# Performance work log

Measured on AMD Instinct MI355X. Metric: run time of the kernel, lower is better.

## Reference

```python
import jax, jax.numpy as jnp
import numpy as np

B, F = 65536, 64
H1, H2 = 64, 64  # linear_layers = [64, 64]
NEG_SLOPE = 0.05


def leaky(x):
    return jnp.where(x >= 0, x, NEG_SLOPE * x)


def setup_inputs() -> dict:
    key = jax.random.key(0)
    ks = jax.random.split(key, 7)
    x = jax.random.normal(ks[0], (B, 1, F), dtype=jnp.float32)
    # Per-feature stacked weights (PyTorch default init scale ~ 1/sqrt(fan_in))
    W1 = jax.random.uniform(ks[1], (F, H1), jnp.float32, -1.0, 1.0)          # Linear(1, H1) weight, fan_in=1
    b1 = jax.random.uniform(ks[2], (F, H1), jnp.float32, -1.0, 1.0)
    s2 = 1.0 / np.sqrt(H1)
    W2 = jax.random.uniform(ks[3], (F, H2, H1), jnp.float32, -s2, s2)        # Linear(H1, H2)
    b2 = jax.random.uniform(ks[4], (F, H2), jnp.float32, -s2, s2)
    s3 = 1.0 / np.sqrt(H2)
    W3 = jax.random.uniform(ks[5], (F, H2), jnp.float32, -s3, s3)            # Linear(H2, 1) weight
    b3 = jax.random.uniform(ks[6], (F,), jnp.float32, -s3, s3)
    return {"x": x, "W1": W1, "b1": b1, "W2": W2, "b2": b2, "W3": W3, "b3": b3}


def reference(x, W1, b1, W2, b2, W3, b3):
    # x: [B, 1, F]; apply an independent tiny 2-layer MLP to each scalar feature.
    xs = x[:, 0, :]                                   # [B, F]
    h = leaky(xs[:, :, None] * W1[None] + b1[None])   # [B, F, H1]
    h = leaky(jnp.einsum('bfh,fgh->bfg', h, W2) + b2[None])  # [B, F, H2]
    y = jnp.einsum('bfg,fg->bf', h, W3) + b3[None]    # [B, F]
    return y[:, None, :]                              # [B, 1, F], same shape as x
```

## Files before the change

kernel.cpp:

```cpp
#include <hip/hip_runtime.h>

typedef _Float16 half8  __attribute__((ext_vector_type(8)));
typedef _Float16 half4v __attribute__((ext_vector_type(4)));
typedef float    floatx4 __attribute__((ext_vector_type(4)));

static constexpr int BR      = 256;
static constexpr int FG      = 16;
static constexpr int XP      = 17;
static constexpr int THREADS = 256;
#define NEG_SLOPE 0.05f

__global__ __launch_bounds__(256)
void w2_half_kernel(const float* __restrict__ W2, _Float16* __restrict__ W2h) {
    int i = (blockIdx.x * 256 + threadIdx.x) * 4;
    floatx4 v = *reinterpret_cast<const floatx4*>(W2 + i);
    half4v h;
    h[0] = (_Float16)v[0]; h[1] = (_Float16)v[1];
    h[2] = (_Float16)v[2]; h[3] = (_Float16)v[3];
    *reinterpret_cast<half4v*>(W2h + i) = h;
}

__global__ __launch_bounds__(THREADS, 3)
void mft_kernel(const float* __restrict__ x,
                const float* __restrict__ W1,
                const float* __restrict__ b1,
                const _Float16* __restrict__ W2h,
                const float* __restrict__ b2,
                const float* __restrict__ W3,
                const float* __restrict__ b3,
                float* __restrict__ y) {
    __shared__ float xl[BR * XP];
    __shared__ float yl[BR * XP];

    const int tid   = threadIdx.x;
    const int fg    = blockIdx.x & 3;
    const int chunk = blockIdx.x >> 2;
    const int gbase = chunk * (BR * 64) + fg * FG;

    #pragma unroll
    for (int k = 0; k < (BR * FG) / (THREADS * 4); ++k) {
        int i  = (k * THREADS + tid) * 4;
        int r  = i >> 4;
        int fi = i & 15;
        floatx4 v = *reinterpret_cast<const floatx4*>(x + gbase + r * 64 + fi);
        xl[r * XP + fi + 0] = v[0];
        xl[r * XP + fi + 1] = v[1];
        xl[r * XP + fi + 2] = v[2];
        xl[r * XP + fi + 3] = v[3];
    }
    __syncthreads();

    const int lane = tid & 63;
    const int wave = tid >> 6;
    const int l15  = lane & 15;
    const int lg   = lane >> 4;

    for (int fi = 0; fi < FG; ++fi) {
        const int f = fg * FG + fi;
        const _Float16* w2f = W2h + f * 4096;

        half8 afrag[4][2];
        #pragma unroll
        for (int m = 0; m < 4; ++m)
            #pragma unroll
            for (int s = 0; s < 2; ++s)
                afrag[m][s] = *reinterpret_cast<const half8*>(
                    w2f + (m * 16 + l15) * 64 + s * 32 + lg * 8);

        floatx4 w1a[2][2], b1a[2][2];
        #pragma unroll
        for (int s = 0; s < 2; ++s) {
            const int ko = s * 32 + lg * 8;
            w1a[s][0] = *reinterpret_cast<const floatx4*>(W1 + f * 64 + ko);
            w1a[s][1] = *reinterpret_cast<const floatx4*>(W1 + f * 64 + ko + 4);
            b1a[s][0] = *reinterpret_cast<const floatx4*>(b1 + f * 64 + ko);
            b1a[s][1] = *reinterpret_cast<const floatx4*>(b1 + f * 64 + ko + 4);
        }
        floatx4 b2a[4], w3a[4];
        #pragma unroll
        for (int m = 0; m < 4; ++m) {
            b2a[m] = *reinterpret_cast<const floatx4*>(b2 + f * 64 + m * 16 + lg * 4);
            w3a[m] = *reinterpret_cast<const floatx4*>(W3 + f * 64 + m * 16 + lg * 4);
        }
        const float b3v = b3[f];

        #pragma unroll
        for (int t = 0; t < 4; ++t) {
            const int r = (wave * 4 + t) * 16 + l15;
            const float xv = xl[r * XP + fi];

            half8 bfrag[2];
            #pragma unroll
            for (int s = 0; s < 2; ++s)
                #pragma unroll
                for (int j = 0; j < 8; ++j) {
                    float v = fmaf(xv, w1a[s][j >> 2][j & 3], b1a[s][j >> 2][j & 3]);
                    v = fmaxf(v, NEG_SLOPE * v);
                    bfrag[s][j] = (_Float16)v;
                }

            float yv = 0.0f;
            #pragma unroll
            for (int m = 0; m < 4; ++m) {
                floatx4 acc = b2a[m];
                acc = __builtin_amdgcn_mfma_f32_16x16x32_f16(afrag[m][0], bfrag[0], acc, 0, 0, 0);
                acc = __builtin_amdgcn_mfma_f32_16x16x32_f16(afrag[m][1], bfrag[1], acc, 0, 0, 0);
                #pragma unroll
                for (int q = 0; q < 4; ++q) {
                    float h2 = acc[q];
                    h2 = fmaxf(h2, NEG_SLOPE * h2);
                    yv = fmaf(h2, w3a[m][q], yv);
                }
            }
            yv += __shfl_xor(yv, 16, 64);
            yv += __shfl_xor(yv, 32, 64);
            if (lane < 16)
                yl[r * XP + fi] = yv + b3v;
        }
    }
    __syncthreads();

    #pragma unroll
    for (int k = 0; k < (BR * FG) / (THREADS * 4); ++k) {
        int i  = (k * THREADS + tid) * 4;
        int r  = i >> 4;
        int fi = i & 15;
        floatx4 v;
        v[0] = yl[r * XP + fi + 0];
        v[1] = yl[r * XP + fi + 1];
        v[2] = yl[r * XP + fi + 2];
        v[3] = yl[r * XP + fi + 3];
        *reinterpret_cast<floatx4*>(y + gbase + r * 64 + fi) = v;
    }
}

extern "C" void kernel_launch(void* const* d_in, const int* in_sizes, int n_in,
                              void* d_out, int out_size, void* d_ws, size_t ws_size,
                              hipStream_t stream) {
    const float* x  = (const float*)d_in[0];
    const float* W1 = (const float*)d_in[1];
    const float* b1 = (const float*)d_in[2];
    const float* W2 = (const float*)d_in[3];
    const float* b2 = (const float*)d_in[4];
    const float* W3 = (const float*)d_in[5];
    const float* b3 = (const float*)d_in[6];
    float*       yo = (float*)d_out;
    _Float16*  W2h  = (_Float16*)d_ws;

    w2_half_kernel<<<dim3(262144 / 1024), dim3(256), 0, stream>>>(W2, W2h);

    const int nblocks = (65536 / BR) * 4;
    mft_kernel<<<dim3(nblocks), dim3(THREADS), 0, stream>>>(
        x, W1, b1, W2h, b2, W3, b3, yo);
}
```

Before: 179.0 us.

## Compute first layer in packed fp16 with pre-converted W1/b1 and x

W1 and b1 are now converted to fp16 in the same packing kernel as W2. x is stored in shared memory as fp16, and the first layer plus leaky-ReLU runs as packed half2 FMA/max. This removes the per-element fp32 FMA and fp32-to-fp16 conversion work that builds the MFMA B operand. Launch bounds are raised to 4 waves-per-EU occupancy and the feature loop is unrolled by 2. In exchange, x, W1 and b1 lose precision before the first-layer arithmetic, which could increase numerical error.

```diff
diff --git a/kernel.cpp b/kernel.cpp
--- a/kernel.cpp
+++ b/kernel.cpp
@@ -2,35 +2,51 @@
 
 typedef _Float16 half8  __attribute__((ext_vector_type(8)));
 typedef _Float16 half4v __attribute__((ext_vector_type(4)));
+typedef _Float16 half2v __attribute__((ext_vector_type(2)));
 typedef float    floatx4 __attribute__((ext_vector_type(4)));
 
 static constexpr int BR      = 256;
 static constexpr int FG      = 16;
-static constexpr int XP      = 17;
+static constexpr int XPH     = 20;
+static constexpr int XPF     = 17;
 static constexpr int THREADS = 256;
 #define NEG_SLOPE 0.05f
 
+static constexpr int W2_OFF     = 0;
+static constexpr int W1_OFF     = 262144;
+static constexpr int B1_OFF     = 266240;
+static constexpr int PACK_TOTAL = 270336;
+
 __global__ __launch_bounds__(256)
-void w2_half_kernel(const float* __restrict__ W2, _Float16* __restrict__ W2h) {
+void pack_kernel(const float* __restrict__ W2, const float* __restrict__ W1,
+                 const float* __restrict__ b1, _Float16* __restrict__ out) {
     int i = (blockIdx.x * 256 + threadIdx.x) * 4;
-    floatx4 v = *reinterpret_cast<const floatx4*>(W2 + i);
+    if (i >= PACK_TOTAL) return;
+    const float* src;
+    int base;
+    if (i < W1_OFF)      { src = W2; base = 0; }
+    else if (i < B1_OFF) { src = W1; base = W1_OFF; }
+    else                 { src = b1; base = B1_OFF; }
+    floatx4 v = *reinterpret_cast<const floatx4*>(src + (i - base));
     half4v h;
     h[0] = (_Float16)v[0]; h[1] = (_Float16)v[1];
     h[2] = (_Float16)v[2]; h[3] = (_Float16)v[3];
-    *reinterpret_cast<half4v*>(W2h + i) = h;
+    *reinterpret_cast<half4v*>(out + i) = h;
 }
 
-__global__ __launch_bounds__(THREADS, 3)
+__global__ __launch_bounds__(THREADS, 4)
 void mft_kernel(const float* __restrict__ x,
-                const float* __restrict__ W1,
-                const float* __restrict__ b1,
-                const _Float16* __restrict__ W2h,
+                const _Float16* __restrict__ wpk,
                 const float* __restrict__ b2,
                 const float* __restrict__ W3,
                 const float* __restrict__ b3,
                 float* __restrict__ y) {
-    __shared__ float xl[BR * XP];
-    __shared__ float yl[BR * XP];
+    __shared__ _Float16 xl[BR * XPH];
+    __shared__ float    yl[BR * XPF];
+
+    const _Float16* __restrict__ W2h = wpk + W2_OFF;
+    const _Float16* __restrict__ W1h = wpk + W1_OFF;
+    const _Float16* __restrict__ B1h = wpk + B1_OFF;
 
     const int tid   = threadIdx.x;
     const int fg    = blockIdx.x & 3;
@@ -43,10 +59,10 @@
         int r  = i >> 4;
         int fi = i & 15;
         floatx4 v = *reinterpret_cast<const floatx4*>(x + gbase + r * 64 + fi);
-        xl[r * XP + fi + 0] = v[0];
-        xl[r * XP + fi + 1] = v[1];
-        xl[r * XP + fi + 2] = v[2];
-        xl[r * XP + fi + 3] = v[3];
+        half4v h;
+        h[0] = (_Float16)v[0]; h[1] = (_Float16)v[1];
+        h[2] = (_Float16)v[2]; h[3] = (_Float16)v[3];
+        *reinterpret_cast<half4v*>(&xl[r * XPH + fi]) = h;
     }
     __syncthreads();
 
@@ -55,6 +71,9 @@
     const int l15  = lane & 15;
     const int lg   = lane >> 4;
 
+    const half2v c005 = {(_Float16)NEG_SLOPE, (_Float16)NEG_SLOPE};
+
+    #pragma unroll 2
     for (int fi = 0; fi < FG; ++fi) {
         const int f = fg * FG + fi;
         const _Float16* w2f = W2h + f * 4096;
@@ -67,14 +86,11 @@
                 afrag[m][s] = *reinterpret_cast<const half8*>(
                     w2f + (m * 16 + l15) * 64 + s * 32 + lg * 8);
 
-        floatx4 w1a[2][2], b1a[2][2];
+        half8 w1c[2], b1c[2];
         #pragma unroll
         for (int s = 0; s < 2; ++s) {
-            const int ko = s * 32 + lg * 8;
-            w1a[s][0] = *reinterpret_cast<const floatx4*>(W1 + f * 64 + ko);
-            w1a[s][1] = *reinterpret_cast<const floatx4*>(W1 + f * 64 + ko + 4);
-            b1a[s][0] = *reinterpret_cast<const floatx4*>(b1 + f * 64 + ko);
-            b1a[s][1] = *reinterpret_cast<const floatx4*>(b1 + f * 64 + ko + 4);
+            w1c[s] = *reinterpret_cast<const half8*>(W1h + f * 64 + s * 32 + lg * 8);
+            b1c[s] = *reinterpret_cast<const half8*>(B1h + f * 64 + s * 32 + lg * 8);
         }
         floatx4 b2a[4], w3a[4];
         #pragma unroll
@@ -87,24 +103,31 @@
         #pragma unroll
         for (int t = 0; t < 4; ++t) {
             const int r = (wave * 4 + t) * 16 + l15;
-            const float xv = xl[r * XP + fi];
+            const _Float16 xh = xl[r * XPH + fi];
+            const half2v x2 = {xh, xh};
 
-            half8 bfrag[2];
+            half8 bf0, bf1;
             #pragma unroll
-            for (int s = 0; s < 2; ++s)
-                #pragma unroll
-                for (int j = 0; j < 8; ++j) {
-                    float v = fmaf(xv, w1a[s][j >> 2][j & 3], b1a[s][j >> 2][j & 3]);
-                    v = fmaxf(v, NEG_SLOPE * v);
-                    bfrag[s][j] = (_Float16)v;
-                }
+            for (int p = 0; p < 4; ++p) {
+                half2v w0 = {w1c[0][2 * p], w1c[0][2 * p + 1]};
+                half2v c0 = {b1c[0][2 * p], b1c[0][2 * p + 1]};
+                half2v h0 = x2 * w0 + c0;
+                half2v r0 = __builtin_elementwise_max(h0, h0 * c005);
+                bf0[2 * p] = r0[0]; bf0[2 * p + 1] = r0[1];
+
+                half2v w1_ = {w1c[1][2 * p], w1c[1][2 * p + 1]};
+                half2v c1 = {b1c[1][2 * p], b1c[1][2 * p + 1]};
+                half2v h1 = x2 * w1_ + c1;
+                half2v r1 = __builtin_elementwise_max(h1, h1 * c005);
+                bf1[2 * p] = r1[0]; bf1[2 * p + 1] = r1[1];
+            }
 
             float yv = 0.0f;
             #pragma unroll
             for (int m = 0; m < 4; ++m) {
                 floatx4 acc = b2a[m];
-                acc = __builtin_amdgcn_mfma_f32_16x16x32_f16(afrag[m][0], bfrag[0], acc, 0, 0, 0);
-                acc = __builtin_amdgcn_mfma_f32_16x16x32_f16(afrag[m][1], bfrag[1], acc, 0, 0, 0);
+                acc = __builtin_amdgcn_mfma_f32_16x16x32_f16(afrag[m][0], bf0, acc, 0, 0, 0);
+                acc = __builtin_amdgcn_mfma_f32_16x16x32_f16(afrag[m][1], bf1, acc, 0, 0, 0);
                 #pragma unroll
                 for (int q = 0; q < 4; ++q) {
                     float h2 = acc[q];
@@ -115,7 +138,7 @@
             yv += __shfl_xor(yv, 16, 64);
             yv += __shfl_xor(yv, 32, 64);
             if (lane < 16)
-                yl[r * XP + fi] = yv + b3v;
+                yl[r * XPF + fi] = yv + b3v;
         }
     }
     __syncthreads();
@@ -126,10 +149,10 @@
         int r  = i >> 4;
         int fi = i & 15;
         floatx4 v;
-        v[0] = yl[r * XP + fi + 0];
-        v[1] = yl[r * XP + fi + 1];
-        v[2] = yl[r * XP + fi + 2];
-        v[3] = yl[r * XP + fi + 3];
+        v[0] = yl[r * XPF + fi + 0];
+        v[1] = yl[r * XPF + fi + 1];
+        v[2] = yl[r * XPF + fi + 2];
+        v[3] = yl[r * XPF + fi + 3];
         *reinterpret_cast<floatx4*>(y + gbase + r * 64 + fi) = v;
     }
 }
@@ -145,11 +168,11 @@
     const float* W3 = (const float*)d_in[5];
     const float* b3 = (const float*)d_in[6];
     float*       yo = (float*)d_out;
-    _Float16*  W2h  = (_Float16*)d_ws;
+    _Float16*   wpk = (_Float16*)d_ws;
 
-    w2_half_kernel<<<dim3(262144 / 1024), dim3(256), 0, stream>>>(W2, W2h);
+    pack_kernel<<<dim3(PACK_TOTAL / 1024), dim3(256), 0, stream>>>(W2, W1, b1, wpk);
 
     const int nblocks = (65536 / BR) * 4;
     mft_kernel<<<dim3(nblocks), dim3(THREADS), 0, stream>>>(
-        x, W1, b1, W2h, b2, W3, b3, yo);
+        x, wpk, b2, W3, b3, yo);
 }
```

Result: faster. 173.8 us (-2.9%).
